# Kernel optimization log

Hardware: AMD Instinct MI355X
Metric: run time of the kernel (lower is better)

## Reference

```python
import jax, jax.numpy as jnp
import numpy as np

NEG_SLOPE = 0.2
EPS = 1e-16


def gat_layer(x, src, dst, W, att_src, att_dst, bias, heads, out_ch, concat, n_nodes):
    # Linear projection -> [N, H, C]
    h = (x @ W).reshape(n_nodes, heads, out_ch)
    # Per-node attention logits [N, H]
    a_src = (h * att_src[None]).sum(-1)
    a_dst = (h * att_dst[None]).sum(-1)
    # Per-edge logits, LeakyReLU (message j -> i with src=j, dst=i)
    alpha = a_src[src] + a_dst[dst]                      # [E, H]
    alpha = jnp.where(alpha >= 0, alpha, NEG_SLOPE * alpha)
    # Segment softmax over incoming edges of each dst node
    amax = jax.ops.segment_max(alpha, dst, num_segments=n_nodes)  # [N, H]
    ealpha = jnp.exp(alpha - amax[dst])
    denom = jax.ops.segment_sum(ealpha, dst, num_segments=n_nodes)
    alpha = ealpha / (denom[dst] + EPS)
    # Weighted messages + scatter-add aggregation
    msg = h[src] * alpha[..., None]                      # [E, H, C]
    out = jax.ops.segment_sum(msg, dst, num_segments=n_nodes)  # [N, H, C]
    out = out.reshape(n_nodes, heads * out_ch) if concat else out.mean(axis=1)
    return out + bias


def setup_inputs() -> dict:
    key = jax.random.key(0)
    ks = jax.random.split(key, 11)
    N, E, F, H, C1 = 50000, 1600000, 128, 8, 8
    x = jax.random.normal(ks[0], (N, F), dtype=jnp.float32)
    edge_index = jax.random.randint(ks[1], (2, E), 0, N, dtype=jnp.int64)
    s = 1.0 / np.sqrt(F)
    W1 = jax.random.normal(ks[2], (F, H * C1), dtype=jnp.float32) * s
    att_src1 = jax.random.normal(ks[3], (H, C1), dtype=jnp.float32) * 0.1
    att_dst1 = jax.random.normal(ks[4], (H, C1), dtype=jnp.float32) * 0.1
    bias1 = jax.random.normal(ks[5], (H * C1,), dtype=jnp.float32) * 0.1
    W2 = jax.random.normal(ks[6], (H * C1, F), dtype=jnp.float32) * (1.0 / np.sqrt(H * C1))
    att_src2 = jax.random.normal(ks[7], (1, F), dtype=jnp.float32) * 0.1
    att_dst2 = jax.random.normal(ks[8], (1, F), dtype=jnp.float32) * 0.1
    bias2 = jax.random.normal(ks[9], (F,), dtype=jnp.float32) * 0.1
    return {"x": x, "edge_index": edge_index, "W1": W1, "att_src1": att_src1,
            "att_dst1": att_dst1, "bias1": bias1, "W2": W2, "att_src2": att_src2,
            "att_dst2": att_dst2, "bias2": bias2}


def reference(x, edge_index, W1, att_src1, att_dst1, bias1, W2, att_src2, att_dst2, bias2):
    N = x.shape[0]
    # PyG GATConv add_self_loops=True: append (i, i) for every node
    loops = jnp.arange(N, dtype=edge_index.dtype)
    src = jnp.concatenate([edge_index[0], loops])
    dst = jnp.concatenate([edge_index[1], loops])
    # eval mode: dropouts are identity
    h = gat_layer(x, src, dst, W1, att_src1, att_dst1, bias1, heads=8, out_ch=8,
                  concat=True, n_nodes=N)            # [N, 64]
    h = jax.nn.elu(h)
    out = gat_layer(h, src, dst, W2, att_src2, att_dst2, bias2, heads=1, out_ch=128,
                    concat=False, n_nodes=N)         # [N, 128]
    return out
```

## Files before the change

kernel.cpp:

```cpp
#include <hip/hip_runtime.h>
#include <stdint.h>

#define NEG_SLOPE 0.2f
#define EPSV 1e-16f
#define LOG2E 1.44269504088896340736f
#define NBLK 256
#define BCAP 12288
#define PKCAP 8192

typedef __attribute__((ext_vector_type(8))) _Float16 half8;
typedef __attribute__((ext_vector_type(4))) float f32x4;

__device__ inline void get_edge(const void* ei, int is64, int E, int e, int& s, int& d){
  if (e >= E){ s = d = e - E; return; }
  if (is64){
    const long long* p = (const long long*)ei;
    s = (int)p[e]; d = (int)p[(long long)E + e];
  } else {
    const int* p = (const int*)ei;
    s = p[e]; d = p[E + e];
  }
}

__device__ inline void pack_one(const float* W, _Float16* Wp, int NCOL, int idx){
  int NNT = NCOL >> 4;
  int j = idx & 7, n16 = (idx >> 3) & 15, q = (idx >> 7) & 3, tile = idx >> 9;
  int nt = tile % NNT, kt = tile / NNT;
  int k = kt*32 + q*8 + j, n = nt*16 + n16;
  Wp[idx] = (_Float16)W[k*NCOL + n];
}

__global__ __launch_bounds__(256) void k1(const void* ei,
                     const float* __restrict__ W1, _Float16* __restrict__ W1p,
                     const float* __restrict__ W2, _Float16* __restrict__ W2p,
                     const float* __restrict__ as2, const float* __restrict__ ad2,
                     float* __restrict__ va_s, float* __restrict__ va_d,
                     int E, int E2,
                     int* __restrict__ gcnt,
                     unsigned* __restrict__ packed){
  __shared__ unsigned pk[PKCAP];
  __shared__ int h[256];
  __shared__ int cur[256];
  int b = blockIdx.x, t = threadIdx.x;
  if (b < 64){
    int idx = b*256 + t;
    if (idx < 8192) pack_one(W1, W1p, 64, idx);
    else            pack_one(W2, W2p, 128, idx - 8192);
    return;
  }
  if (b == 64){
    if (t < 64){
      float s = 0.f, d = 0.f;
      for (int c = 0; c < 128; ++c){
        float w = W2[t*128 + c];
        s = fmaf(w, as2[c], s);
        d = fmaf(w, ad2[c], d);
      }
      va_s[t] = s * LOG2E; va_d[t] = d * LOG2E;
    }
    return;
  }
  int blk = b - 65;
  int chunk = (E2 + NBLK - 1)/NBLK;
  int beg = blk*chunk, end = min(beg + chunk, E2), cnt = end - beg;
  const int* e32 = (const int*)ei;
  int nz = 0;
  for (int i = 0; i < 64; ++i) nz |= e32[2*i + 1];
  int is64 = (nz == 0) ? 1 : 0;
  h[t] = 0; __syncthreads();
  for (int j = t; j < cnt; j += 256){
    int s, d; get_edge(ei, is64, E, beg + j, s, d);
    unsigned p = ((unsigned)s << 16) | (unsigned)d;
    pk[j] = p;
    atomicAdd(&h[(p >> 8) & 255u], 1);
  }
  __syncthreads();
  int mine = h[t];
  int base_t = 0;
  if (mine > 0) base_t = atomicAdd(&gcnt[t*16], mine);
  cur[t] = base_t;
  __syncthreads();
  for (int j = t; j < cnt; j += 256){
    unsigned p = pk[j];
    int bk = (p >> 8) & 255u;
    int pos = atomicAdd(&cur[bk], 1);
    packed[(size_t)bk*BCAP + pos] = p;
  }
}

__global__ __launch_bounds__(256) void gemm1(const float* __restrict__ x, const _Float16* __restrict__ Bp,
                                             const float* __restrict__ att_s, const float* __restrict__ att_d,
                                             _Float16* __restrict__ Cb,
                                             float* __restrict__ asrc1, float* __restrict__ adst1, int M){
  constexpr int NKT = 4, NNT = 4;
  int wave = (blockIdx.x*256 + (int)threadIdx.x) >> 6;
  int lane = threadIdx.x & 63;
  int row0 = wave << 4;
  if (row0 >= M) return;
  int m = lane & 15, q = lane >> 4;
  f32x4 acc[NNT];
#pragma unroll
  for (int i = 0; i < NNT; ++i) acc[i] = (f32x4){0.f,0.f,0.f,0.f};
#pragma unroll
  for (int kt = 0; kt < NKT; ++kt){
    const float* xr = x + (size_t)(row0 + m)*128 + kt*32 + q*8;
    f32x4 f0 = *(const f32x4*)xr;
    f32x4 f1 = *(const f32x4*)(xr + 4);
    half8 a;
#pragma unroll
    for (int j = 0; j < 4; ++j){ a[j] = (_Float16)f0[j]; a[4 + j] = (_Float16)f1[j]; }
#pragma unroll
    for (int nt = 0; nt < NNT; ++nt){
      half8 b = *(const half8*)(Bp + (size_t)(((kt*NNT + nt)*4 + q)*16 + m)*8);
      acc[nt] = __builtin_amdgcn_mfma_f32_16x16x32_f16(a, b, acc[nt], 0, 0, 0);
    }
  }
#pragma unroll
  for (int nt = 0; nt < NNT; ++nt){
#pragma unroll
    for (int r = 0; r < 4; ++r){
      Cb[(size_t)(row0 + q*4 + r)*64 + nt*16 + m] = (_Float16)acc[nt][r];
    }
  }
  float atts[4], attd[4];
#pragma unroll
  for (int nt = 0; nt < 4; ++nt){
    atts[nt] = att_s[nt*16 + m] * LOG2E;
    attd[nt] = att_d[nt*16 + m] * LOG2E;
  }
  int isw = (m & 7) == 0;
#pragma unroll
  for (int r = 0; r < 4; ++r){
    int row = row0 + q*4 + r;
#pragma unroll
    for (int nt = 0; nt < 4; ++nt){
      float ps = acc[nt][r] * atts[nt];
      float pd = acc[nt][r] * attd[nt];
#pragma unroll
      for (int mm = 1; mm <= 4; mm <<= 1){
        ps += __shfl_xor(ps, mm, 64);
        pd += __shfl_xor(pd, mm, 64);
      }
      if (isw){
        int head = 2*nt + (m >> 3);
        asrc1[row*8 + head] = ps;
        adst1[row*8 + head] = pd;
      }
    }
  }
}

__global__ __launch_bounds__(256) void gemm2(const _Float16* __restrict__ A, const _Float16* __restrict__ Bp,
                                             const float* __restrict__ bias,
                                             float* __restrict__ C, int M){
  constexpr int NKT = 2, NNT = 8;
  int wave = (blockIdx.x*256 + (int)threadIdx.x) >> 6;
  int lane = threadIdx.x & 63;
  int row0 = wave << 4;
  if (row0 >= M) return;
  int m = lane & 15, q = lane >> 4;
  f32x4 acc[NNT];
#pragma unroll
  for (int i = 0; i < NNT; ++i) acc[i] = (f32x4){0.f,0.f,0.f,0.f};
#pragma unroll
  for (int kt = 0; kt < NKT; ++kt){
    half8 a = *(const half8*)(A + (size_t)(row0 + m)*64 + kt*32 + q*8);
#pragma unroll
    for (int nt = 0; nt < NNT; ++nt){
      half8 b = *(const half8*)(Bp + (size_t)(((kt*NNT + nt)*4 + q)*16 + m)*8);
      acc[nt] = __builtin_amdgcn_mfma_f32_16x16x32_f16(a, b, acc[nt], 0, 0, 0);
    }
  }
#pragma unroll
  for (int nt = 0; nt < NNT; ++nt){
    float bv = bias[nt*16 + m];
#pragma unroll
    for (int r = 0; r < 4; ++r){
      C[(size_t)(row0 + q*4 + r)*128 + nt*16 + m] = acc[nt][r] + bv;
    }
  }
}

__global__ __launch_bounds__(256) void p4_sort(const unsigned* __restrict__ packed,
                                               const int* __restrict__ gcnt,
                                               int N, int E2,
                                               int* __restrict__ offs, int* __restrict__ srcs){
  __shared__ int hist[256];
  __shared__ int cur[256];
  __shared__ int tot[256];
  __shared__ int sbase, scnt;
  int b = blockIdx.x, t = threadIdx.x;
  int v0 = gcnt[t*16];
  tot[t] = v0; __syncthreads();
  for (int off = 1; off < 256; off <<= 1){
    int v = (t >= off) ? tot[t - off] : 0;
    __syncthreads(); tot[t] += v; __syncthreads();
  }
  if (t == b){ sbase = tot[t] - v0; scnt = v0; }
  __syncthreads();
  int base = sbase, cnt = scnt;
  hist[t] = 0; __syncthreads();
  const unsigned* bp = packed + (size_t)b*BCAP;
  for (int p = t; p < cnt; p += 256){
    atomicAdd(&hist[bp[p] & 255u], 1);
  }
  __syncthreads();
  int v = hist[t];
  cur[t] = v; __syncthreads();
  for (int off = 1; off < 256; off <<= 1){
    int u = (t >= off) ? cur[t - off] : 0;
    __syncthreads(); cur[t] += u; __syncthreads();
  }
  int ex = cur[t] - v;
  __syncthreads();
  cur[t] = ex;
  int node = b*256 + t;
  if (node < N) offs[node] = base + ex;
  __syncthreads();
  for (int p = t; p < cnt; p += 256){
    unsigned pk = bp[p];
    int pos = atomicAdd(&cur[pk & 255u], 1);
    srcs[base + pos] = (int)((pk >> 16) << 7);
  }
  if (b == 0 && t == 0) offs[N] = E2;
}

__global__ __launch_bounds__(256) void agg_l1(const char* __restrict__ h1b,
                       const float* __restrict__ asrc, const float* __restrict__ adst,
                       const int* __restrict__ offs, const int* __restrict__ srcs,
                       const float* __restrict__ bias,
                       const float* __restrict__ va_s, const float* __restrict__ va_d,
                       uint4* __restrict__ hout,
                       float* __restrict__ asrc2, float* __restrict__ adst2, int N){
  int tid = threadIdx.x;
  int i = blockIdx.x*4 + (tid >> 6);
  if (i >= N) return;
  int lane = tid & 63, g = lane >> 3, c = lane & 7;
  unsigned coff = (unsigned)(c << 4);
  float ad = adst[i*8 + c];
  int beg = offs[i], end = offs[i + 1], last = end - 1;
  float acc[8];
#pragma unroll
  for (int k = 0; k < 8; ++k) acc[k] = 0.f;
  float den = 0.f;
  for (int p = beg; p < end; p += 32){
    int m[4]; unsigned so[4];
#pragma unroll
    for (int k = 0; k < 4; ++k) m[k] = p + 8*k + g;
#pragma unroll
    for (int k = 0; k < 4; ++k) so[k] = (unsigned)srcs[min(m[k], last)];
    float a[4];
#pragma unroll
    for (int k = 0; k < 4; ++k) a[k] = asrc[(so[k] >> 4) + (unsigned)c];
    half8 v[4];
#pragma unroll
    for (int k = 0; k < 4; ++k) v[k] = *(const half8*)(h1b + (size_t)(so[k] + coff));
    float w[4];
#pragma unroll
    for (int k = 0; k < 4; ++k){
      float z = a[k] + ad;
      z = fmaxf(z, NEG_SLOPE*z);
      w[k] = (m[k] < end) ? exp2f(z) : 0.f;
      den += w[k];
    }
#pragma unroll
    for (int k = 0; k < 4; ++k){
#pragma unroll
      for (int j = 0; j < 8; ++j){
        acc[j] = fmaf((float)v[k][j], w[k], acc[j]);
      }
    }
  }
#pragma unroll
  for (int mm = 8; mm <= 32; mm <<= 1){
#pragma unroll
    for (int k = 0; k < 8; ++k) acc[k] += __shfl_xor(acc[k], mm, 64);
    den += __shfl_xor(den, mm, 64);
  }
  if (g == 0){
    float inv = 1.f/(den + EPSV);
    float o[8];
    union { _Float16 h[8]; uint4 u; } ov;
#pragma unroll
    for (int k = 0; k < 8; ++k){
      float t = acc[k]*inv + bias[c*8 + k];
      t = (t > 0.f) ? t : (__expf(t) - 1.f);
      o[k] = t;
      ov.h[k] = (_Float16)t;
    }
    hout[(size_t)i*8 + c] = ov.u;
    float ps = 0.f, pd = 0.f;
#pragma unroll
    for (int k = 0; k < 8; ++k){
      ps = fmaf(o[k], va_s[c*8 + k], ps);
      pd = fmaf(o[k], va_d[c*8 + k], pd);
    }
#pragma unroll
    for (int mm = 1; mm <= 4; mm <<= 1){
      ps += __shfl_xor(ps, mm, 8);
      pd += __shfl_xor(pd, mm, 8);
    }
    if (c == 0){ asrc2[i] = ps; adst2[i] = pd; }
  }
}

__global__ __launch_bounds__(256) void agg_l2(const char* __restrict__ hin2,
                       const float* __restrict__ asrc, const float* __restrict__ adst,
                       const int* __restrict__ offs, const int* __restrict__ srcs,
                       uint4* __restrict__ qout, int N){
  int tid = threadIdx.x;
  int i = blockIdx.x*4 + (tid >> 6);
  if (i >= N) return;
  int lane = tid & 63, g = lane >> 3, c = lane & 7;
  unsigned coff = (unsigned)(c << 4);
  float ad = adst[i];
  int beg = offs[i], end = offs[i + 1], last = end - 1;
  float acc[8];
#pragma unroll
  for (int k = 0; k < 8; ++k) acc[k] = 0.f;
  float den = 0.f;
  for (int p = beg; p < end; p += 32){
    int m[4]; unsigned so[4];
#pragma unroll
    for (int k = 0; k < 4; ++k) m[k] = p + 8*k + g;
#pragma unroll
    for (int k = 0; k < 4; ++k) so[k] = (unsigned)srcs[min(m[k], last)];
    float a[4];
#pragma unroll
    for (int k = 0; k < 4; ++k) a[k] = asrc[so[k] >> 7];
    half8 v[4];
#pragma unroll
    for (int k = 0; k < 4; ++k) v[k] = *(const half8*)(hin2 + (size_t)(so[k] + coff));
    float w[4];
#pragma unroll
    for (int k = 0; k < 4; ++k){
      float z = a[k] + ad;
      z = fmaxf(z, NEG_SLOPE*z);
      w[k] = (m[k] < end) ? exp2f(z) : 0.f;
      den += w[k];
    }
#pragma unroll
    for (int k = 0; k < 4; ++k){
#pragma unroll
      for (int j = 0; j < 8; ++j){
        acc[j] = fmaf((float)v[k][j], w[k], acc[j]);
      }
    }
  }
#pragma unroll
  for (int mm = 8; mm <= 32; mm <<= 1){
#pragma unroll
    for (int k = 0; k < 8; ++k) acc[k] += __shfl_xor(acc[k], mm, 64);
    den += __shfl_xor(den, mm, 64);
  }
  if (g == 0){
    float inv = 1.f/(den + EPSV);
    union { _Float16 h[8]; uint4 u; } ov;
#pragma unroll
    for (int k = 0; k < 8; ++k) ov.h[k] = (_Float16)(acc[k]*inv);
    qout[(size_t)i*8 + c] = ov.u;
  }
}

extern "C" void kernel_launch(void* const* d_in, const int* in_sizes, int n_in,
                              void* d_out, int out_size, void* d_ws, size_t ws_size,
                              hipStream_t stream){
  const float* x   = (const float*)d_in[0];
  const void*  ei  = d_in[1];
  const float* W1  = (const float*)d_in[2];
  const float* as1 = (const float*)d_in[3];
  const float* ad1 = (const float*)d_in[4];
  const float* b1  = (const float*)d_in[5];
  const float* W2  = (const float*)d_in[6];
  const float* as2 = (const float*)d_in[7];
  const float* ad2 = (const float*)d_in[8];
  const float* b2  = (const float*)d_in[9];

  int N  = in_sizes[0] / 128;
  int E  = in_sizes[1] / 2;
  int E2 = E + N;
  int NB = (N + 255) >> 8;

  char* p = (char*)d_ws;
  auto alloc = [&](size_t bytes) -> void* {
    void* r = (void*)p;
    p += (bytes + 255) & ~(size_t)255;
    return r;
  };
  _Float16* W1p    = (_Float16*)alloc((size_t)128*64*2);
  _Float16* W2p    = (_Float16*)alloc((size_t)64*128*2);
  _Float16* h1b    = (_Float16*)alloc((size_t)N*64*2);
  float*    asrc1  = (float*)alloc((size_t)N*8*4);
  float*    adst1  = (float*)alloc((size_t)N*8*4);
  _Float16* hin2   = (_Float16*)alloc((size_t)N*64*2);
  _Float16* hq     = (_Float16*)alloc((size_t)N*64*2);
  float*    asrc2  = (float*)alloc((size_t)N*4);
  float*    adst2  = (float*)alloc((size_t)N*4);
  float*    va_s2  = (float*)alloc(64*4);
  float*    va_d2  = (float*)alloc(64*4);
  int*      offs   = (int*)alloc((size_t)(N + 1)*4);
  int*      srcs   = (int*)alloc((size_t)E2*4);
  unsigned* packed = (unsigned*)alloc((size_t)256*BCAP*4);
  int*      gcnt   = (int*)alloc((size_t)256*16*4);

  dim3 B(256);
  hipMemsetAsync(gcnt, 0, (size_t)256*16*4, stream);

  k1<<<65 + NBLK, B, 0, stream>>>(ei, W1, W1p, W2, W2p, as2, ad2, va_s2, va_d2,
                                  E, E2, gcnt, packed);

  int nwav = (N + 15)/16;
  gemm1<<<(nwav + 3)/4, B, 0, stream>>>(x, W1p, as1, ad1, h1b, asrc1, adst1, N);

  p4_sort<<<NB, B, 0, stream>>>(packed, gcnt, N, E2, offs, srcs);

  agg_l1<<<(N + 3)/4, B, 0, stream>>>((const char*)h1b, asrc1, adst1, offs, srcs, b1,
                                      va_s2, va_d2, (uint4*)hin2, asrc2, adst2, N);

  agg_l2<<<(N + 3)/4, B, 0, stream>>>((const char*)hin2, asrc2, adst2, offs, srcs,
                                      (uint4*)hq, N);

  gemm2<<<(nwav + 3)/4, B, 0, stream>>>(hq, W2p, b2, (float*)d_out, N);
}
```

Measured before the change: 223.6 us.

## Fuse gemm1 into edge-bucketing kernel and software-prefetch gathers in aggregation loops

Merges the layer-1 GEMM into the first kernel. Each GEMM block now packs W1 into fp16 in shared memory itself, so the separate W1 packing pass and the gemm1 launch go away and the GEMM runs alongside the edge bucketing blocks. Both aggregation kernels now double-buffer the next batch of src indices, attention logits and feature loads before computing the current batch, to hide gather latency. The cost is that every GEMM block repacks W1 redundantly, the shared-memory footprint grows to 34KB for all blocks, and the prefetch adds register pressure.

```diff
diff --git a/kernel.cpp b/kernel.cpp
--- a/kernel.cpp
+++ b/kernel.cpp
@@ -22,33 +22,99 @@
   }
 }
 
-__device__ inline void pack_one(const float* W, _Float16* Wp, int NCOL, int idx){
-  int NNT = NCOL >> 4;
-  int j = idx & 7, n16 = (idx >> 3) & 15, q = (idx >> 7) & 3, tile = idx >> 9;
-  int nt = tile % NNT, kt = tile / NNT;
-  int k = kt*32 + q*8 + j, n = nt*16 + n16;
-  Wp[idx] = (_Float16)W[k*NCOL + n];
-}
-
-__global__ __launch_bounds__(256) void k1(const void* ei,
-                     const float* __restrict__ W1, _Float16* __restrict__ W1p,
+__global__ __launch_bounds__(256) void k1g(const void* ei,
+                     const float* __restrict__ x,
+                     const float* __restrict__ W1,
+                     const float* __restrict__ att_s, const float* __restrict__ att_d,
+                     _Float16* __restrict__ Cb,
+                     float* __restrict__ asrc1, float* __restrict__ adst1, int M,
                      const float* __restrict__ W2, _Float16* __restrict__ W2p,
                      const float* __restrict__ as2, const float* __restrict__ ad2,
                      float* __restrict__ va_s, float* __restrict__ va_d,
-                     int E, int E2,
+                     int E, int E2, int GG,
                      int* __restrict__ gcnt,
                      unsigned* __restrict__ packed){
-  __shared__ unsigned pk[PKCAP];
-  __shared__ int h[256];
-  __shared__ int cur[256];
+  __shared__ char smem[34*1024];
   int b = blockIdx.x, t = threadIdx.x;
-  if (b < 64){
-    int idx = b*256 + t;
-    if (idx < 8192) pack_one(W1, W1p, 64, idx);
-    else            pack_one(W2, W2p, 128, idx - 8192);
+
+  if (b < GG){
+    _Float16* Bs = (_Float16*)smem;
+#pragma unroll
+    for (int r = 0; r < 32; ++r){
+      int idx = r*256 + t;
+      int j = idx & 7, n16 = (idx >> 3) & 15, q = (idx >> 7) & 3, tile = idx >> 9;
+      int nt = tile & 3, kt = tile >> 2;
+      int k = kt*32 + q*8 + j, n = nt*16 + n16;
+      Bs[idx] = (_Float16)W1[k*64 + n];
+    }
+    __syncthreads();
+    int wave = (b*256 + t) >> 6;
+    int lane = t & 63;
+    int row0 = wave << 4;
+    if (row0 >= M) return;
+    int m = lane & 15, q = lane >> 4;
+    f32x4 acc[4];
+#pragma unroll
+    for (int i = 0; i < 4; ++i) acc[i] = (f32x4){0.f,0.f,0.f,0.f};
+#pragma unroll
+    for (int kt = 0; kt < 4; ++kt){
+      const float* xr = x + (size_t)(row0 + m)*128 + kt*32 + q*8;
+      f32x4 f0 = *(const f32x4*)xr;
+      f32x4 f1 = *(const f32x4*)(xr + 4);
+      half8 a;
+#pragma unroll
+      for (int j = 0; j < 4; ++j){ a[j] = (_Float16)f0[j]; a[4 + j] = (_Float16)f1[j]; }
+#pragma unroll
+      for (int nt = 0; nt < 4; ++nt){
+        half8 bfr = *(const half8*)(Bs + (size_t)(((kt*4 + nt)*4 + q)*16 + m)*8);
+        acc[nt] = __builtin_amdgcn_mfma_f32_16x16x32_f16(a, bfr, acc[nt], 0, 0, 0);
+      }
+    }
+#pragma unroll
+    for (int nt = 0; nt < 4; ++nt){
+#pragma unroll
+      for (int r = 0; r < 4; ++r){
+        Cb[(size_t)(row0 + q*4 + r)*64 + nt*16 + m] = (_Float16)acc[nt][r];
+      }
+    }
+    float atts[4], attd[4];
+#pragma unroll
+    for (int nt = 0; nt < 4; ++nt){
+      atts[nt] = att_s[nt*16 + m] * LOG2E;
+      attd[nt] = att_d[nt*16 + m] * LOG2E;
+    }
+    int isw = (m & 7) == 0;
+#pragma unroll
+    for (int r = 0; r < 4; ++r){
+      int row = row0 + q*4 + r;
+#pragma unroll
+      for (int nt = 0; nt < 4; ++nt){
+        float ps = acc[nt][r] * atts[nt];
+        float pd = acc[nt][r] * attd[nt];
+#pragma unroll
+        for (int mm = 1; mm <= 4; mm <<= 1){
+          ps += __shfl_xor(ps, mm, 64);
+          pd += __shfl_xor(pd, mm, 64);
+        }
+        if (isw){
+          int head = 2*nt + (m >> 3);
+          asrc1[row*8 + head] = ps;
+          adst1[row*8 + head] = pd;
+        }
+      }
+    }
     return;
   }
-  if (b == 64){
+
+  if (b == GG){
+#pragma unroll
+    for (int r = 0; r < 32; ++r){
+      int idx = r*256 + t;
+      int j = idx & 7, n16 = (idx >> 3) & 15, q = (idx >> 7) & 3, tile = idx >> 9;
+      int nt = tile & 7, kt = tile >> 3;
+      int k = kt*32 + q*8 + j, n = nt*16 + n16;
+      W2p[idx] = (_Float16)W2[k*128 + n];
+    }
     if (t < 64){
       float s = 0.f, d = 0.f;
       for (int c = 0; c < 128; ++c){
@@ -60,7 +126,11 @@
     }
     return;
   }
-  int blk = b - 65;
+
+  unsigned* pk = (unsigned*)smem;
+  int* h   = (int*)(smem + 32*1024);
+  int* cur = (int*)(smem + 33*1024);
+  int blk = b - GG - 1;
   int chunk = (E2 + NBLK - 1)/NBLK;
   int beg = blk*chunk, end = min(beg + chunk, E2), cnt = end - beg;
   const int* e32 = (const int*)ei;
@@ -85,68 +155,6 @@
     int bk = (p >> 8) & 255u;
     int pos = atomicAdd(&cur[bk], 1);
     packed[(size_t)bk*BCAP + pos] = p;
-  }
-}
-
-__global__ __launch_bounds__(256) void gemm1(const float* __restrict__ x, const _Float16* __restrict__ Bp,
-                                             const float* __restrict__ att_s, const float* __restrict__ att_d,
-                                             _Float16* __restrict__ Cb,
-                                             float* __restrict__ asrc1, float* __restrict__ adst1, int M){
-  constexpr int NKT = 4, NNT = 4;
-  int wave = (blockIdx.x*256 + (int)threadIdx.x) >> 6;
-  int lane = threadIdx.x & 63;
-  int row0 = wave << 4;
-  if (row0 >= M) return;
-  int m = lane & 15, q = lane >> 4;
-  f32x4 acc[NNT];
-#pragma unroll
-  for (int i = 0; i < NNT; ++i) acc[i] = (f32x4){0.f,0.f,0.f,0.f};
-#pragma unroll
-  for (int kt = 0; kt < NKT; ++kt){
-    const float* xr = x + (size_t)(row0 + m)*128 + kt*32 + q*8;
-    f32x4 f0 = *(const f32x4*)xr;
-    f32x4 f1 = *(const f32x4*)(xr + 4);
-    half8 a;
-#pragma unroll
-    for (int j = 0; j < 4; ++j){ a[j] = (_Float16)f0[j]; a[4 + j] = (_Float16)f1[j]; }
-#pragma unroll
-    for (int nt = 0; nt < NNT; ++nt){
-      half8 b = *(const half8*)(Bp + (size_t)(((kt*NNT + nt)*4 + q)*16 + m)*8);
-      acc[nt] = __builtin_amdgcn_mfma_f32_16x16x32_f16(a, b, acc[nt], 0, 0, 0);
-    }
-  }
-#pragma unroll
-  for (int nt = 0; nt < NNT; ++nt){
-#pragma unroll
-    for (int r = 0; r < 4; ++r){
-      Cb[(size_t)(row0 + q*4 + r)*64 + nt*16 + m] = (_Float16)acc[nt][r];
-    }
-  }
-  float atts[4], attd[4];
-#pragma unroll
-  for (int nt = 0; nt < 4; ++nt){
-    atts[nt] = att_s[nt*16 + m] * LOG2E;
-    attd[nt] = att_d[nt*16 + m] * LOG2E;
-  }
-  int isw = (m & 7) == 0;
-#pragma unroll
-  for (int r = 0; r < 4; ++r){
-    int row = row0 + q*4 + r;
-#pragma unroll
-    for (int nt = 0; nt < 4; ++nt){
-      float ps = acc[nt][r] * atts[nt];
-      float pd = acc[nt][r] * attd[nt];
-#pragma unroll
-      for (int mm = 1; mm <= 4; mm <<= 1){
-        ps += __shfl_xor(ps, mm, 64);
-        pd += __shfl_xor(pd, mm, 64);
-      }
-      if (isw){
-        int head = 2*nt + (m >> 3);
-        asrc1[row*8 + head] = ps;
-        adst1[row*8 + head] = pd;
-      }
-    }
   }
 }
 
@@ -243,24 +251,31 @@
 #pragma unroll
   for (int k = 0; k < 8; ++k) acc[k] = 0.f;
   float den = 0.f;
+  float a[4]; half8 v[4];
+  {
+    unsigned so[4];
+#pragma unroll
+    for (int k = 0; k < 4; ++k) so[k] = (unsigned)srcs[min(beg + 8*k + g, last)];
+#pragma unroll
+    for (int k = 0; k < 4; ++k) a[k] = asrc[(so[k] >> 4) + (unsigned)c];
+#pragma unroll
+    for (int k = 0; k < 4; ++k) v[k] = *(const half8*)(h1b + (size_t)(so[k] + coff));
+  }
   for (int p = beg; p < end; p += 32){
-    int m[4]; unsigned so[4];
-#pragma unroll
-    for (int k = 0; k < 4; ++k) m[k] = p + 8*k + g;
-#pragma unroll
-    for (int k = 0; k < 4; ++k) so[k] = (unsigned)srcs[min(m[k], last)];
-    float a[4];
-#pragma unroll
-    for (int k = 0; k < 4; ++k) a[k] = asrc[(so[k] >> 4) + (unsigned)c];
-    half8 v[4];
-#pragma unroll
-    for (int k = 0; k < 4; ++k) v[k] = *(const half8*)(h1b + (size_t)(so[k] + coff));
+    int pn = p + 32;
+    unsigned so_n[4]; float a_n[4]; half8 v_n[4];
+#pragma unroll
+    for (int k = 0; k < 4; ++k) so_n[k] = (unsigned)srcs[min(pn + 8*k + g, last)];
+#pragma unroll
+    for (int k = 0; k < 4; ++k) a_n[k] = asrc[(so_n[k] >> 4) + (unsigned)c];
+#pragma unroll
+    for (int k = 0; k < 4; ++k) v_n[k] = *(const half8*)(h1b + (size_t)(so_n[k] + coff));
     float w[4];
 #pragma unroll
     for (int k = 0; k < 4; ++k){
       float z = a[k] + ad;
       z = fmaxf(z, NEG_SLOPE*z);
-      w[k] = (m[k] < end) ? exp2f(z) : 0.f;
+      w[k] = (p + 8*k + g < end) ? exp2f(z) : 0.f;
       den += w[k];
     }
 #pragma unroll
@@ -270,6 +285,8 @@
         acc[j] = fmaf((float)v[k][j], w[k], acc[j]);
       }
     }
+#pragma unroll
+    for (int k = 0; k < 4; ++k){ a[k] = a_n[k]; v[k] = v_n[k]; }
   }
 #pragma unroll
   for (int mm = 8; mm <= 32; mm <<= 1){
@@ -319,24 +336,31 @@
 #pragma unroll
   for (int k = 0; k < 8; ++k) acc[k] = 0.f;
   float den = 0.f;
+  float a[4]; half8 v[4];
+  {
+    unsigned so[4];
+#pragma unroll
+    for (int k = 0; k < 4; ++k) so[k] = (unsigned)srcs[min(beg + 8*k + g, last)];
+#pragma unroll
+    for (int k = 0; k < 4; ++k) a[k] = asrc[so[k] >> 7];
+#pragma unroll
+    for (int k = 0; k < 4; ++k) v[k] = *(const half8*)(hin2 + (size_t)(so[k] + coff));
+  }
   for (int p = beg; p < end; p += 32){
-    int m[4]; unsigned so[4];
-#pragma unroll
-    for (int k = 0; k < 4; ++k) m[k] = p + 8*k + g;
-#pragma unroll
-    for (int k = 0; k < 4; ++k) so[k] = (unsigned)srcs[min(m[k], last)];
-    float a[4];
-#pragma unroll
-    for (int k = 0; k < 4; ++k) a[k] = asrc[so[k] >> 7];
-    half8 v[4];
-#pragma unroll
-    for (int k = 0; k < 4; ++k) v[k] = *(const half8*)(hin2 + (size_t)(so[k] + coff));
+    int pn = p + 32;
+    unsigned so_n[4]; float a_n[4]; half8 v_n[4];
+#pragma unroll
+    for (int k = 0; k < 4; ++k) so_n[k] = (unsigned)srcs[min(pn + 8*k + g, last)];
+#pragma unroll
+    for (int k = 0; k < 4; ++k) a_n[k] = asrc[so_n[k] >> 7];
+#pragma unroll
+    for (int k = 0; k < 4; ++k) v_n[k] = *(const half8*)(hin2 + (size_t)(so_n[k] + coff));
     float w[4];
 #pragma unroll
     for (int k = 0; k < 4; ++k){
       float z = a[k] + ad;
       z = fmaxf(z, NEG_SLOPE*z);
-      w[k] = (m[k] < end) ? exp2f(z) : 0.f;
+      w[k] = (p + 8*k + g < end) ? exp2f(z) : 0.f;
       den += w[k];
     }
 #pragma unroll
@@ -346,6 +370,8 @@
         acc[j] = fmaf((float)v[k][j], w[k], acc[j]);
       }
     }
+#pragma unroll
+    for (int k = 0; k < 4; ++k){ a[k] = a_n[k]; v[k] = v_n[k]; }
   }
 #pragma unroll
   for (int mm = 8; mm <= 32; mm <<= 1){
@@ -387,7 +413,6 @@
     p += (bytes + 255) & ~(size_t)255;
     return r;
   };
-  _Float16* W1p    = (_Float16*)alloc((size_t)128*64*2);
   _Float16* W2p    = (_Float16*)alloc((size_t)64*128*2);
   _Float16* h1b    = (_Float16*)alloc((size_t)N*64*2);
   float*    asrc1  = (float*)alloc((size_t)N*8*4);
@@ -406,11 +431,12 @@
   dim3 B(256);
   hipMemsetAsync(gcnt, 0, (size_t)256*16*4, stream);
 
-  k1<<<65 + NBLK, B, 0, stream>>>(ei, W1, W1p, W2, W2p, as2, ad2, va_s2, va_d2,
-                                  E, E2, gcnt, packed);
-
   int nwav = (N + 15)/16;
-  gemm1<<<(nwav + 3)/4, B, 0, stream>>>(x, W1p, as1, ad1, h1b, asrc1, adst1, N);
+  int GG = (nwav + 3)/4;
+
+  k1g<<<GG + 1 + NBLK, B, 0, stream>>>(ei, x, W1, as1, ad1, h1b, asrc1, adst1, N,
+                                       W2, W2p, as2, ad2, va_s2, va_d2,
+                                       E, E2, GG, gcnt, packed);
 
   p4_sort<<<NB, B, 0, stream>>>(packed, gcnt, N, E2, offs, srcs);
 
```

Result: slower. 240.7 us (+7.6%).
